# Optimization experiments

Measured on AMD Instinct MI355X. Metric: run time of the kernel, lower is better.

## Reference

```python
import jax, jax.numpy as jnp
import numpy as np

B, S = 2, 1024          # 2 sequences of 1024 tokens (prefill)
HID = 2880
HQ, HKV, D = 64, 8, 64  # query heads, kv heads, head_dim
W = 128                 # sliding window size
THETA = 150000.0
SCALE = D ** -0.5
Q_SIZE, KV_SIZE = HQ * D, HKV * D


def _rope_neox(pos, x):
    # pos: [T] int, x: [T, H, D] -> neox-style full-dim rotary
    half = D // 2
    inv_freq = 1.0 / (THETA ** (jnp.arange(half, dtype=jnp.float32) * 2.0 / D))
    ang = pos.astype(jnp.float32)[:, None] * inv_freq          # [T, D/2]
    cos = jnp.cos(ang)[:, None, :]                             # [T, 1, D/2]
    sin = jnp.sin(ang)[:, None, :]
    x1, x2 = x[..., :half], x[..., half:]
    return jnp.concatenate([x1 * cos - x2 * sin, x1 * sin + x2 * cos], axis=-1)


def setup_inputs() -> dict:
    key = jax.random.key(0)
    ks = jax.random.split(key, 10)
    s = 0.02
    hidden_states = jax.random.normal(ks[0], (B * S, HID), dtype=jnp.float32)
    positions = jnp.tile(jnp.arange(S, dtype=jnp.int32), B)    # per-sequence positions
    Wq = jax.random.normal(ks[1], (HID, Q_SIZE), dtype=jnp.float32) * s
    bq = jax.random.normal(ks[2], (Q_SIZE,), dtype=jnp.float32) * s
    Wk = jax.random.normal(ks[3], (HID, KV_SIZE), dtype=jnp.float32) * s
    bk = jax.random.normal(ks[4], (KV_SIZE,), dtype=jnp.float32) * s
    Wv = jax.random.normal(ks[5], (HID, KV_SIZE), dtype=jnp.float32) * s
    bv = jax.random.normal(ks[6], (KV_SIZE,), dtype=jnp.float32) * s
    Wo = jax.random.normal(ks[7], (Q_SIZE, HID), dtype=jnp.float32) * s
    bo = jax.random.normal(ks[8], (HID,), dtype=jnp.float32) * s
    return {"hidden_states": hidden_states, "positions": positions,
            "Wq": Wq, "bq": bq, "Wk": Wk, "bk": bk,
            "Wv": Wv, "bv": bv, "Wo": Wo, "bo": bo}


def reference(hidden_states, positions, Wq, bq, Wk, bk, Wv, bv, Wo, bo):
    T = hidden_states.shape[0]
    q = (hidden_states @ Wq + bq).reshape(T, HQ, D)
    k = (hidden_states @ Wk + bk).reshape(T, HKV, D)
    v = (hidden_states @ Wv + bv).reshape(T, HKV, D)
    q = _rope_neox(positions, q)
    k = _rope_neox(positions, k)

    # sliding-window causal attention (banded, window = last W keys + self)
    G = HQ // HKV  # GQA group size
    q5 = q.reshape(B, S, HKV, G, D)
    k4 = k.reshape(B, S, HKV, D)
    v4 = v.reshape(B, S, HKV, D)
    offs = jnp.arange(W + 1)
    idx = jnp.arange(S)[:, None] - W + offs[None, :]           # [S, W+1] key index j
    valid = idx >= 0                                           # causal+window band
    idx_c = jnp.clip(idx, 0, S - 1)
    kw = k4[:, idx_c]                                          # [B, S, W+1, HKV, D]
    vw = v4[:, idx_c]
    scores = jnp.einsum('bikgd,biwkd->bikgw', q5, kw) * SCALE  # [B,S,HKV,G,W+1]
    scores = jnp.where(valid[None, :, None, None, :], scores, jnp.float32(-1e30))
    p = jax.nn.softmax(scores, axis=-1)
    o = jnp.einsum('bikgw,biwkd->bikgd', p, vw).reshape(T, Q_SIZE)
    return o @ Wo + bo


if __name__ == '__main__':
    out = reference(**setup_inputs())
    print(out.shape, out.dtype)
```

## Files before the change

kernel.cpp:

```cpp
#include <hip/hip_runtime.h>

#define T_TOK 2048
#define S_LEN 1024
#define HIDN  2880
#define NHQ   64
#define NHKV  8
#define DH    64
#define QSZ   4096
#define KVSZ  512
#define WIN   128
#define NQKV  5120
#define NOPAD 2944

typedef __attribute__((ext_vector_type(4))) float f32x4;
typedef __attribute__((ext_vector_type(8))) short bf16x8;
typedef __attribute__((ext_vector_type(4))) short s16x4;

__device__ __forceinline__ unsigned short f2bf(float f) {
  unsigned u = __float_as_uint(f);
  u += 0x7fffu + ((u >> 16) & 1u);
  return (unsigned short)(u >> 16);
}
__device__ __forceinline__ float bf2f(unsigned short s) {
  return __uint_as_float(((unsigned)s) << 16);
}
__device__ __forceinline__ void ld_g2l16(const void* g, void* l) {
  __builtin_amdgcn_global_load_lds(
      (const __attribute__((address_space(1))) unsigned int*)g,
      (__attribute__((address_space(3))) unsigned int*)l, 16, 0, 0);
}

#define NB_CONV 2880
#define NB_WQ   5760
#define NB_WK   720

__device__ __forceinline__ void transpose_tile(
    const float* __restrict__ W, unsigned short* __restrict__ WT,
    int N, int lbid, float (*tile)[72])
{
  const int tid = threadIdx.x;
  const int nbx = N >> 6;
  const int nb = (lbid % nbx) * 64;
  const int kb = (lbid / nbx) * 32;
  const int kk = tid >> 3;
  const int n8 = (tid & 7) * 8;
  const float* src = W + (size_t)(kb + kk) * N + nb + n8;
  *(f32x4*)&tile[kk][n8]     = *(const f32x4*)(src);
  *(f32x4*)&tile[kk][n8 + 4] = *(const f32x4*)(src + 4);
  __syncthreads();
  const int n  = tid & 63;
  const int k8 = (tid >> 6) * 8;
  bf16x8 p;
  #pragma unroll
  for (int j = 0; j < 8; ++j) p[j] = (short)f2bf(tile[k8 + j][n]);
  *(bf16x8*)(WT + (size_t)(nb + n) * HIDN + kb + k8) = p;
}

__global__ __launch_bounds__(256) void prep_kernel(
    const float* __restrict__ hidden, unsigned short* __restrict__ hbf,
    const float* __restrict__ Wq, const float* __restrict__ Wk,
    const float* __restrict__ Wv, unsigned short* __restrict__ WT)
{
  __shared__ float tile[32][72];
  const int bid = blockIdx.x;
  if (bid < NB_CONV) {
    const size_t off = ((size_t)bid * 256 + threadIdx.x) * 8;
    const f32x4 a = *(const f32x4*)(hidden + off);
    const f32x4 b = *(const f32x4*)(hidden + off + 4);
    bf16x8 p;
    p[0] = (short)f2bf(a[0]); p[1] = (short)f2bf(a[1]);
    p[2] = (short)f2bf(a[2]); p[3] = (short)f2bf(a[3]);
    p[4] = (short)f2bf(b[0]); p[5] = (short)f2bf(b[1]);
    p[6] = (short)f2bf(b[2]); p[7] = (short)f2bf(b[3]);
    *(bf16x8*)(hbf + off) = p;
  } else if (bid < NB_CONV + NB_WQ) {
    transpose_tile(Wq, WT, QSZ, bid - NB_CONV, tile);
  } else if (bid < NB_CONV + NB_WQ + NB_WK) {
    transpose_tile(Wk, WT + (size_t)QSZ * HIDN, KVSZ,
                   bid - NB_CONV - NB_WQ, tile);
  } else {
    transpose_tile(Wv, WT + (size_t)(QSZ + KVSZ) * HIDN, KVSZ,
                   bid - NB_CONV - NB_WQ - NB_WK, tile);
  }
}

__global__ __launch_bounds__(256) void transpose_w(
    const float* __restrict__ W, unsigned short* __restrict__ WT,
    int K, int N)
{
  __shared__ float tile[32][72];
  const int tid = threadIdx.x;
  const int nb = blockIdx.x * 64;
  const int kb = blockIdx.y * 32;
  const int kk = tid >> 3;
  const int n8 = (tid & 7) * 8;
  if (nb + 64 <= N) {
    const float* src = W + (size_t)(kb + kk) * N + nb + n8;
    *(f32x4*)&tile[kk][n8]     = *(const f32x4*)(src);
    *(f32x4*)&tile[kk][n8 + 4] = *(const f32x4*)(src + 4);
  } else {
    #pragma unroll
    for (int u = 0; u < 8; ++u)
      tile[kk][n8 + u] = (nb + n8 + u < N)
          ? W[(size_t)(kb + kk) * N + nb + n8 + u] : 0.f;
  }
  __syncthreads();
  const int n  = tid & 63;
  const int k8 = (tid >> 6) * 8;
  bf16x8 p;
  #pragma unroll
  for (int j = 0; j < 8; ++j) p[j] = (short)f2bf(tile[k8 + j][n]);
  *(bf16x8*)(WT + (size_t)(nb + n) * K + kb + k8) = p;
}

__device__ __forceinline__ void rope_epilogue(
    f32x4 acc[4][4], const float* __restrict__ bias,
    const int* __restrict__ pos, unsigned short* __restrict__ outp,
    int outStride, int colbase, int rowbase, int lane)
{
  const int fr = lane & 15;
  const int r4 = (lane >> 4) * 4;
  const float invf0 = exp2f((float)fr        * (-17.19460283f / 32.0f));
  const float invf1 = exp2f((float)(fr + 16) * (-17.19460283f / 32.0f));
  #pragma unroll
  for (int mt = 0; mt < 4; ++mt) {
    #pragma unroll
    for (int i = 0; i < 4; ++i) {
      const int m = rowbase + mt * 16 + r4 + i;
      const float p = (float)pos[m];
      #pragma unroll
      for (int ntp = 0; ntp < 2; ++ntp) {
        float sv, cv;
        __sincosf(p * (ntp ? invf1 : invf0), &sv, &cv);
        const int c1 = colbase + ntp * 16 + fr;
        const float x1 = acc[mt][ntp][i]     + bias[c1];
        const float x2 = acc[mt][ntp + 2][i] + bias[c1 + 32];
        outp[(size_t)m * outStride + c1]      = f2bf(x1 * cv - x2 * sv);
        outp[(size_t)m * outStride + c1 + 32] = f2bf(x1 * sv + x2 * cv);
      }
    }
  }
}

__global__ __launch_bounds__(256) void gemm_qkv(
    const unsigned short* __restrict__ A, const unsigned short* __restrict__ BT,
    const float* __restrict__ bq, const float* __restrict__ bk,
    const float* __restrict__ bv, const int* __restrict__ pos,
    unsigned short* __restrict__ qb, unsigned short* __restrict__ kb,
    unsigned short* __restrict__ vT)
{
  __shared__ unsigned short As[128 * 64];
  __shared__ unsigned short Bs[128 * 64];
  const int tid  = threadIdx.x;
  const int lane = tid & 63;
  const int wid  = tid >> 6;
  const int wr   = (wid >> 1) * 64;
  const int wc   = (wid & 1) * 64;
  const int m0 = blockIdx.y * 128;
  const int n0 = blockIdx.x * 128;
  const int fr = lane & 15;
  const int fq = lane >> 4;

  f32x4 acc[4][4];
  #pragma unroll
  for (int i = 0; i < 4; ++i)
    #pragma unroll
    for (int j = 0; j < 4; ++j) acc[i][j] = (f32x4){0.f, 0.f, 0.f, 0.f};

  const int rsub = tid >> 3;
  const int cg   = (tid & 7) ^ (rsub & 7);
  const unsigned short* Ap = A  + (size_t)(m0 + rsub) * HIDN + cg * 8;
  const unsigned short* Bp = BT + (size_t)(n0 + rsub) * HIDN + cg * 8;
  const size_t rstep = (size_t)32 * HIDN;

  for (int k0 = 0; k0 < HIDN; k0 += 64) {
    #pragma unroll
    for (int i = 0; i < 4; ++i)
      ld_g2l16(Ap + i * rstep + k0, As + ((size_t)i * 256 + tid) * 8);
    #pragma unroll
    for (int i = 0; i < 4; ++i)
      ld_g2l16(Bp + i * rstep + k0, Bs + ((size_t)i * 256 + tid) * 8);
    __syncthreads();
    #pragma unroll
    for (int ks = 0; ks < 2; ++ks) {
      const int kc = ks * 4 + fq;
      bf16x8 af[4], bfr[4];
      #pragma unroll
      for (int mt = 0; mt < 4; ++mt) {
        const int R = wr + mt * 16 + fr;
        af[mt] = *(const bf16x8*)(As + R * 64 + ((kc ^ (R & 7)) << 3));
      }
      #pragma unroll
      for (int nt = 0; nt < 4; ++nt) {
        const int R = wc + nt * 16 + fr;
        bfr[nt] = *(const bf16x8*)(Bs + R * 64 + ((kc ^ (R & 7)) << 3));
      }
      #pragma unroll
      for (int mt = 0; mt < 4; ++mt)
        #pragma unroll
        for (int nt = 0; nt < 4; ++nt)
          acc[mt][nt] = __builtin_amdgcn_mfma_f32_16x16x32_bf16(
              af[mt], bfr[nt], acc[mt][nt], 0, 0, 0);
    }
    __syncthreads();
  }

  const int r4 = (lane >> 4) * 4;
  if (n0 < QSZ) {
    rope_epilogue(acc, bq, pos, qb, QSZ, n0 + wc, m0 + wr, lane);
  } else if (n0 < QSZ + KVSZ) {
    rope_epilogue(acc, bk, pos, kb, KVSZ, n0 - QSZ + wc, m0 + wr, lane);
  } else {
    #pragma unroll
    for (int nt = 0; nt < 4; ++nt) {
      const int vrow = n0 - (QSZ + KVSZ) + wc + nt * 16 + fr;
      const float bvv = bv[vrow];
      #pragma unroll
      for (int mt = 0; mt < 4; ++mt) {
        const int mb = m0 + wr + mt * 16 + r4;
        s16x4 p;
        p[0] = (short)f2bf(acc[mt][nt][0] + bvv);
        p[1] = (short)f2bf(acc[mt][nt][1] + bvv);
        p[2] = (short)f2bf(acc[mt][nt][2] + bvv);
        p[3] = (short)f2bf(acc[mt][nt][3] + bvv);
        *(s16x4*)(vT + (size_t)vrow * T_TOK + mb) = p;
      }
    }
  }
}

__global__ __launch_bounds__(256) void gemm_o(
    const unsigned short* __restrict__ A, const unsigned short* __restrict__ BT,
    const float* __restrict__ bias, float* __restrict__ C)
{
  __shared__ unsigned short As[128 * 64];
  __shared__ unsigned short Bs[128 * 64];
  const int tid  = threadIdx.x;
  const int lane = tid & 63;
  const int wid  = tid >> 6;
  const int wr   = (wid >> 1) * 64;
  const int wc   = (wid & 1) * 64;
  const int m0 = blockIdx.y * 128;
  const int n0 = blockIdx.x * 128;
  const int fr = lane & 15;
  const int fq = lane >> 4;

  f32x4 acc[4][4];
  #pragma unroll
  for (int i = 0; i < 4; ++i)
    #pragma unroll
    for (int j = 0; j < 4; ++j) acc[i][j] = (f32x4){0.f, 0.f, 0.f, 0.f};

  const int rsub = tid >> 3;
  const int cg   = (tid & 7) ^ (rsub & 7);
  const unsigned short* Ap = A  + (size_t)(m0 + rsub) * QSZ + cg * 8;
  const unsigned short* Bp = BT + (size_t)(n0 + rsub) * QSZ + cg * 8;
  const size_t rstep = (size_t)32 * QSZ;

  for (int k0 = 0; k0 < QSZ; k0 += 64) {
    #pragma unroll
    for (int i = 0; i < 4; ++i)
      ld_g2l16(Ap + i * rstep + k0, As + ((size_t)i * 256 + tid) * 8);
    #pragma unroll
    for (int i = 0; i < 4; ++i)
      ld_g2l16(Bp + i * rstep + k0, Bs + ((size_t)i * 256 + tid) * 8);
    __syncthreads();
    #pragma unroll
    for (int ks = 0; ks < 2; ++ks) {
      const int kc = ks * 4 + fq;
      bf16x8 af[4], bfr[4];
      #pragma unroll
      for (int mt = 0; mt < 4; ++mt) {
        const int R = wr + mt * 16 + fr;
        af[mt] = *(const bf16x8*)(As + R * 64 + ((kc ^ (R & 7)) << 3));
      }
      #pragma unroll
      for (int nt = 0; nt < 4; ++nt) {
        const int R = wc + nt * 16 + fr;
        bfr[nt] = *(const bf16x8*)(Bs + R * 64 + ((kc ^ (R & 7)) << 3));
      }
      #pragma unroll
      for (int mt = 0; mt < 4; ++mt)
        #pragma unroll
        for (int nt = 0; nt < 4; ++nt)
          acc[mt][nt] = __builtin_amdgcn_mfma_f32_16x16x32_bf16(
              af[mt], bfr[nt], acc[mt][nt], 0, 0, 0);
    }
    __syncthreads();
  }

  const int r4 = (lane >> 4) * 4;
  #pragma unroll
  for (int nt = 0; nt < 4; ++nt) {
    const int n = n0 + wc + nt * 16 + fr;
    if (n >= HIDN) continue;
    const float bvv = bias[n];
    #pragma unroll
    for (int mt = 0; mt < 4; ++mt) {
      const int mb = m0 + wr + mt * 16 + r4;
      #pragma unroll
      for (int i = 0; i < 4; ++i)
        C[(size_t)(mb + i) * HIDN + n] = acc[mt][nt][i] + bvv;
    }
  }
}

__global__ __launch_bounds__(256, 3) void attn_kernel(
    const unsigned short* __restrict__ q, const unsigned short* __restrict__ k,
    const unsigned short* __restrict__ vT, unsigned short* __restrict__ o)
{
  __shared__ unsigned short lds[26624];
  unsigned short* Ks = lds;
  unsigned short* Vt = lds;
  unsigned short* Ps = lds + 13824;

  const int tid  = threadIdx.x;
  const int lane = tid & 63;
  const int wid  = tid >> 6;
  const int sq0  = blockIdx.x * 64;
  const int hp   = blockIdx.y;
  const int b    = blockIdx.z;
  const int h0   = hp * 2;
  const int kvh  = hp >> 2;
  const int kp0  = sq0 - WIN;

  const int fr = lane & 15;
  const int fk = (lane >> 4) * 8;
  const int qw = wid * 16;

  bf16x8 qf[2][2];
  {
    const size_t qrow = (size_t)(b * S_LEN + sq0 + qw + fr) * QSZ;
    #pragma unroll
    for (int hh = 0; hh < 2; ++hh)
      #pragma unroll
      for (int ks2 = 0; ks2 < 2; ++ks2)
        qf[hh][ks2] = *(const bf16x8*)(q + qrow + (h0 + hh) * DH + ks2 * 32 + fk);
  }

  #pragma unroll
  for (int j = 0; j < 6; ++j) {
    const int c  = tid + j * 256;
    const int kr = c >> 3, dc = (c & 7) * 8;
    int tok = b * S_LEN + kp0 + kr;
    if (tok < 0) tok = 0;
    const bf16x8 vv = *(const bf16x8*)(k + (size_t)tok * KVSZ + kvh * DH + dc);
    *(bf16x8*)&Ks[kr * 72 + dc] = vv;
  }
  __syncthreads();

  f32x4 S0[12], S1[12];
  #pragma unroll
  for (int i = 0; i < 12; ++i) {
    S0[i] = (f32x4){0.f, 0.f, 0.f, 0.f};
    S1[i] = (f32x4){0.f, 0.f, 0.f, 0.f};
  }
  #pragma unroll
  for (int ks2 = 0; ks2 < 2; ++ks2) {
    #pragma unroll
    for (int nt = 0; nt < 12; ++nt) {
      const bf16x8 bfr = *(const bf16x8*)&Ks[(nt * 16 + fr) * 72 + ks2 * 32 + fk];
      S0[nt] = __builtin_amdgcn_mfma_f32_16x16x32_bf16(qf[0][ks2], bfr, S0[nt], 0, 0, 0);
      S1[nt] = __builtin_amdgcn_mfma_f32_16x16x32_bf16(qf[1][ks2], bfr, S1[nt], 0, 0, 0);
    }
  }

  const int qbase = sq0 + qw + ((lane >> 4) << 2);
  float ls0[4] = {0.f, 0.f, 0.f, 0.f};
  float ls1[4] = {0.f, 0.f, 0.f, 0.f};
  #pragma unroll
  for (int nt = 0; nt < 12; ++nt) {
    const int jpos = kp0 + nt * 16 + fr;
    #pragma unroll
    for (int i = 0; i < 4; ++i) {
      const int qa = qbase + i;
      const bool valid = (jpos >= 0) && (jpos <= qa) && (jpos >= qa - WIN);
      const float e0 = valid ? __expf(S0[nt][i] * 0.125f) : 0.f;
      const float e1 = valid ? __expf(S1[nt][i] * 0.125f) : 0.f;
      S0[nt][i] = e0; ls0[i] += e0;
      S1[nt][i] = e1; ls1[i] += e1;
    }
  }
  #pragma unroll
  for (int off = 1; off < 16; off <<= 1)
    #pragma unroll
    for (int i = 0; i < 4; ++i) {
      ls0[i] += __shfl_xor(ls0[i], off, 64);
      ls1[i] += __shfl_xor(ls1[i], off, 64);
    }
  float inv0[4], inv1[4];
  #pragma unroll
  for (int i = 0; i < 4; ++i) {
    inv0[i] = 1.0f / ls0[i];
    inv1[i] = 1.0f / ls1[i];
  }
  __syncthreads();

  #pragma unroll
  for (int nt = 0; nt < 12; ++nt)
    #pragma unroll
    for (int i = 0; i < 4; ++i)
      Ps[(qbase - sq0 + i) * 200 + nt * 16 + fr] = f2bf(S0[nt][i]);
  if (kp0 >= 0) {
    #pragma unroll
    for (int j = 0; j < 6; ++j) {
      const int c  = tid + j * 256;
      const int dr = c / 24, kc = (c % 24) * 8;
      const bf16x8 vv = *(const bf16x8*)(
          vT + (size_t)(kvh * DH + dr) * T_TOK + b * S_LEN + kp0 + kc);
      *(bf16x8*)&Vt[dr * 200 + kc] = vv;
    }
  } else {
    #pragma unroll
    for (int j = 0; j < 6; ++j) {
      const int c  = tid + j * 256;
      const int dr = c / 24, kc = (c % 24) * 8;
      bf16x8 vv;
      #pragma unroll
      for (int u = 0; u < 8; ++u) {
        int col = b * S_LEN + kp0 + kc + u;
        if (col < 0) col = 0;
        vv[u] = (short)vT[(size_t)(kvh * DH + dr) * T_TOK + col];
      }
      *(bf16x8*)&Vt[dr * 200 + kc] = vv;
    }
  }
  __syncthreads();

  {
    f32x4 O[4];
    #pragma unroll
    for (int i = 0; i < 4; ++i) O[i] = (f32x4){0.f, 0.f, 0.f, 0.f};
    #pragma unroll
    for (int ks2 = 0; ks2 < 6; ++ks2) {
      const bf16x8 pa = *(const bf16x8*)&Ps[(qw + fr) * 200 + ks2 * 32 + fk];
      #pragma unroll
      for (int nt = 0; nt < 4; ++nt) {
        const bf16x8 vb = *(const bf16x8*)&Vt[(nt * 16 + fr) * 200 + ks2 * 32 + fk];
        O[nt] = __builtin_amdgcn_mfma_f32_16x16x32_bf16(pa, vb, O[nt], 0, 0, 0);
      }
    }
    #pragma unroll
    for (int nt = 0; nt < 4; ++nt)
      #pragma unroll
      for (int i = 0; i < 4; ++i)
        o[(size_t)(b * S_LEN + qbase + i) * QSZ + h0 * DH + nt * 16 + fr] =
            f2bf(O[nt][i] * inv0[i]);
  }
  __syncthreads();

  #pragma unroll
  for (int nt = 0; nt < 12; ++nt)
    #pragma unroll
    for (int i = 0; i < 4; ++i)
      Ps[(qbase - sq0 + i) * 200 + nt * 16 + fr] = f2bf(S1[nt][i]);
  __syncthreads();

  {
    f32x4 O[4];
    #pragma unroll
    for (int i = 0; i < 4; ++i) O[i] = (f32x4){0.f, 0.f, 0.f, 0.f};
    #pragma unroll
    for (int ks2 = 0; ks2 < 6; ++ks2) {
      const bf16x8 pa = *(const bf16x8*)&Ps[(qw + fr) * 200 + ks2 * 32 + fk];
      #pragma unroll
      for (int nt = 0; nt < 4; ++nt) {
        const bf16x8 vb = *(const bf16x8*)&Vt[(nt * 16 + fr) * 200 + ks2 * 32 + fk];
        O[nt] = __builtin_amdgcn_mfma_f32_16x16x32_bf16(pa, vb, O[nt], 0, 0, 0);
      }
    }
    #pragma unroll
    for (int nt = 0; nt < 4; ++nt)
      #pragma unroll
      for (int i = 0; i < 4; ++i)
        o[(size_t)(b * S_LEN + qbase + i) * QSZ + (h0 + 1) * DH + nt * 16 + fr] =
            f2bf(O[nt][i] * inv1[i]);
  }
}

extern "C" void kernel_launch(void* const* d_in, const int* in_sizes, int n_in,
                              void* d_out, int out_size, void* d_ws, size_t ws_size,
                              hipStream_t stream) {
  const float* hidden    = (const float*)d_in[0];
  const int*   positions = (const int*)d_in[1];
  const float* Wq = (const float*)d_in[2];
  const float* bq = (const float*)d_in[3];
  const float* Wk = (const float*)d_in[4];
  const float* bk = (const float*)d_in[5];
  const float* Wv = (const float*)d_in[6];
  const float* bv = (const float*)d_in[7];
  const float* Wo = (const float*)d_in[8];
  const float* bo = (const float*)d_in[9];
  float* out = (float*)d_out;

  char* ws = (char*)d_ws;
  unsigned short* hbf   = (unsigned short*)(ws);
  unsigned short* WqkvT = (unsigned short*)(ws + 11796480);
  unsigned short* qb    = (unsigned short*)(ws + 41287680);
  unsigned short* kb    = (unsigned short*)(ws + 58064896);
  unsigned short* vTb   = (unsigned short*)(ws + 60162048);

  prep_kernel<<<dim3(NB_CONV + NB_WQ + 2 * NB_WK), dim3(256), 0, stream>>>(
      hidden, hbf, Wq, Wk, Wv, WqkvT);

  gemm_qkv<<<dim3(NQKV / 128, T_TOK / 128), dim3(256), 0, stream>>>(
      hbf, WqkvT, bq, bk, bv, positions, qb, kb, vTb);

  transpose_w<<<dim3(NOPAD / 64, QSZ / 32), dim3(256), 0, stream>>>(
      Wo, WqkvT, QSZ, HIDN);

  attn_kernel<<<dim3(S_LEN / 64, NHQ / 2, 2), dim3(256), 0, stream>>>(
      qb, kb, vTb, qb);
  gemm_o<<<dim3(NOPAD / 128, T_TOK / 128), dim3(256), 0, stream>>>(
      qb, WqkvT, bo, out);
}
```

Baseline: 375.0 us.

## Rewrite QKV GEMM as 256x256 tile, 8-wave, double-buffered pipelined kernel

```diff
diff --git a/kernel.cpp b/kernel.cpp
--- a/kernel.cpp
+++ b/kernel.cpp
@@ -11,6 +11,7 @@
 #define WIN   128
 #define NQKV  5120
 #define NOPAD 2944
+#define NT    45
 
 typedef __attribute__((ext_vector_type(4))) float f32x4;
 typedef __attribute__((ext_vector_type(8))) short bf16x8;
@@ -113,8 +114,8 @@
   *(bf16x8*)(WT + (size_t)(nb + n) * K + kb + k8) = p;
 }
 
-__device__ __forceinline__ void rope_epilogue(
-    f32x4 acc[4][4], const float* __restrict__ bias,
+__device__ __forceinline__ void rope_epilogue8(
+    f32x4 (*acc)[4], const float* __restrict__ bias,
     const int* __restrict__ pos, unsigned short* __restrict__ outp,
     int outStride, int colbase, int rowbase, int lane)
 {
@@ -123,7 +124,7 @@
   const float invf0 = exp2f((float)fr        * (-17.19460283f / 32.0f));
   const float invf1 = exp2f((float)(fr + 16) * (-17.19460283f / 32.0f));
   #pragma unroll
-  for (int mt = 0; mt < 4; ++mt) {
+  for (int mt = 0; mt < 8; ++mt) {
     #pragma unroll
     for (int i = 0; i < 4; ++i) {
       const int m = rowbase + mt * 16 + r4 + i;
@@ -142,82 +143,128 @@
   }
 }
 
-__global__ __launch_bounds__(256) void gemm_qkv(
+__global__ __launch_bounds__(512, 2) void gemm_qkv(
     const unsigned short* __restrict__ A, const unsigned short* __restrict__ BT,
     const float* __restrict__ bq, const float* __restrict__ bk,
     const float* __restrict__ bv, const int* __restrict__ pos,
     unsigned short* __restrict__ qb, unsigned short* __restrict__ kb,
     unsigned short* __restrict__ vT)
 {
-  __shared__ unsigned short As[128 * 64];
-  __shared__ unsigned short Bs[128 * 64];
+  __shared__ unsigned short lds[65536];
   const int tid  = threadIdx.x;
   const int lane = tid & 63;
   const int wid  = tid >> 6;
-  const int wr   = (wid >> 1) * 64;
-  const int wc   = (wid & 1) * 64;
-  const int m0 = blockIdx.y * 128;
-  const int n0 = blockIdx.x * 128;
+  const int wm   = wid >> 2;
+  const int wn   = wid & 3;
+  const int bid  = blockIdx.x;
+  const int wg   = (bid & 7) * 20 + (bid >> 3);
+  const int n0   = (wg % 20) * 256;
+  const int m0   = (wg / 20) * 256;
   const int fr = lane & 15;
   const int fq = lane >> 4;
 
-  f32x4 acc[4][4];
-  #pragma unroll
-  for (int i = 0; i < 4; ++i)
-    #pragma unroll
-    for (int j = 0; j < 4; ++j) acc[i][j] = (f32x4){0.f, 0.f, 0.f, 0.f};
-
   const int rsub = tid >> 3;
   const int cg   = (tid & 7) ^ (rsub & 7);
-  const unsigned short* Ap = A  + (size_t)(m0 + rsub) * HIDN + cg * 8;
-  const unsigned short* Bp = BT + (size_t)(n0 + rsub) * HIDN + cg * 8;
-  const size_t rstep = (size_t)32 * HIDN;
-
-  for (int k0 = 0; k0 < HIDN; k0 += 64) {
-    #pragma unroll
-    for (int i = 0; i < 4; ++i)
-      ld_g2l16(Ap + i * rstep + k0, As + ((size_t)i * 256 + tid) * 8);
-    #pragma unroll
-    for (int i = 0; i < 4; ++i)
-      ld_g2l16(Bp + i * rstep + k0, Bs + ((size_t)i * 256 + tid) * 8);
-    __syncthreads();
-    #pragma unroll
-    for (int ks = 0; ks < 2; ++ks) {
-      const int kc = ks * 4 + fq;
-      bf16x8 af[4], bfr[4];
-      #pragma unroll
-      for (int mt = 0; mt < 4; ++mt) {
-        const int R = wr + mt * 16 + fr;
-        af[mt] = *(const bf16x8*)(As + R * 64 + ((kc ^ (R & 7)) << 3));
-      }
-      #pragma unroll
-      for (int nt = 0; nt < 4; ++nt) {
-        const int R = wc + nt * 16 + fr;
-        bfr[nt] = *(const bf16x8*)(Bs + R * 64 + ((kc ^ (R & 7)) << 3));
-      }
-      #pragma unroll
-      for (int mt = 0; mt < 4; ++mt)
+  const unsigned short* Asrc = A  + (size_t)(m0 + rsub) * HIDN + cg * 8;
+  const unsigned short* Bsrc = BT + (size_t)(n0 + rsub) * HIDN + cg * 8;
+  const size_t half_step = (size_t)128 * HIDN;
+  const size_t r64 = (size_t)64 * HIDN;
+
+  #define STAGE(src, slot)                                         \
+    do {                                                           \
+      ld_g2l16((src),       (slot) + (size_t)tid * 8);             \
+      ld_g2l16((src) + r64, (slot) + (size_t)(512 + tid) * 8);     \
+    } while (0)
+
+  STAGE(Bsrc,                  lds + 16384);
+  STAGE(Bsrc + half_step,      lds + 24576);
+  STAGE(Asrc,                  lds + 0);
+  STAGE(Asrc + half_step,      lds + 8192);
+  STAGE(Bsrc + 64,             lds + 32768 + 16384);
+  STAGE(Bsrc + half_step + 64, lds + 32768 + 24576);
+  STAGE(Asrc + 64,             lds + 32768 + 0);
+  STAGE(Asrc + half_step + 64, lds + 32768 + 8192);
+  asm volatile("s_waitcnt vmcnt(8)" ::: "memory");
+  __builtin_amdgcn_s_barrier();
+
+  f32x4 acc[8][4];
+  #pragma unroll
+  for (int i = 0; i < 8; ++i)
+    #pragma unroll
+    for (int j = 0; j < 4; ++j) acc[i][j] = (f32x4){0.f, 0.f, 0.f, 0.f};
+  bf16x8 bfr[4][2];
+
+  for (int t = 0; t < NT; ++t) {
+    unsigned short* Abuf = lds + (t & 1) * 32768;
+    unsigned short* Bbuf = Abuf + 16384;
+    unsigned short* nAbuf = lds + ((t + 1) & 1) * 32768;
+    const int kA = (t + 1) * 64;
+    const int kB = (t + 2) * 64;
+    #pragma unroll
+    for (int q = 0; q < 4; ++q) {
+      if (q == 0) {
         #pragma unroll
-        for (int nt = 0; nt < 4; ++nt)
-          acc[mt][nt] = __builtin_amdgcn_mfma_f32_16x16x32_bf16(
-              af[mt], bfr[nt], acc[mt][nt], 0, 0, 0);
-    }
-    __syncthreads();
-  }
-
-  const int r4 = (lane >> 4) * 4;
-  if (n0 < QSZ) {
-    rope_epilogue(acc, bq, pos, qb, QSZ, n0 + wc, m0 + wr, lane);
-  } else if (n0 < QSZ + KVSZ) {
-    rope_epilogue(acc, bk, pos, kb, KVSZ, n0 - QSZ + wc, m0 + wr, lane);
+        for (int nf = 0; nf < 4; ++nf)
+          #pragma unroll
+          for (int ks = 0; ks < 2; ++ks) {
+            const int R = wn * 64 + nf * 16 + fr;
+            const int kc = ks * 4 + fq;
+            bfr[nf][ks] = *(const bf16x8*)(Bbuf + R * 64 + ((kc ^ (R & 7)) << 3));
+          }
+      }
+      bf16x8 af[2][2];
+      #pragma unroll
+      for (int j = 0; j < 2; ++j)
+        #pragma unroll
+        for (int ks = 0; ks < 2; ++ks) {
+          const int R = wm * 128 + (q * 2 + j) * 16 + fr;
+          const int kc = ks * 4 + fq;
+          af[j][ks] = *(const bf16x8*)(Abuf + R * 64 + ((kc ^ (R & 7)) << 3));
+        }
+      if (q == 0) {
+        if (t >= 1 && t <= NT - 2) STAGE(Asrc + kA, nAbuf);
+      } else if (q == 1) {
+        if (t >= 1 && t <= NT - 2) STAGE(Asrc + half_step + kA, nAbuf + 8192);
+      } else if (q == 2) {
+        if (t <= NT - 3) STAGE(Bsrc + kB, Bbuf);
+      } else {
+        if (t <= NT - 3) STAGE(Bsrc + half_step + kB, Bbuf + 8192);
+      }
+      if (q == 3) {
+        if (t < NT - 2)       asm volatile("s_waitcnt vmcnt(4)" ::: "memory");
+        else if (t == NT - 2) asm volatile("s_waitcnt vmcnt(0)" ::: "memory");
+      }
+      __builtin_amdgcn_s_barrier();
+      __builtin_amdgcn_s_setprio(1);
+      #pragma unroll
+      for (int j = 0; j < 2; ++j)
+        #pragma unroll
+        for (int nf = 0; nf < 4; ++nf)
+          #pragma unroll
+          for (int ks = 0; ks < 2; ++ks)
+            acc[q * 2 + j][nf] = __builtin_amdgcn_mfma_f32_16x16x32_bf16(
+                af[j][ks], bfr[nf][ks], acc[q * 2 + j][nf], 0, 0, 0);
+      __builtin_amdgcn_s_setprio(0);
+      __builtin_amdgcn_s_barrier();
+    }
+  }
+  #undef STAGE
+
+  const int cb = n0 + wn * 64;
+  const int rowbase = m0 + wm * 128;
+  if (cb < QSZ) {
+    rope_epilogue8(acc, bq, pos, qb, QSZ, cb, rowbase, lane);
+  } else if (cb < QSZ + KVSZ) {
+    rope_epilogue8(acc, bk, pos, kb, KVSZ, cb - QSZ, rowbase, lane);
   } else {
+    const int r4 = (lane >> 4) * 4;
     #pragma unroll
     for (int nt = 0; nt < 4; ++nt) {
-      const int vrow = n0 - (QSZ + KVSZ) + wc + nt * 16 + fr;
+      const int vrow = cb - (QSZ + KVSZ) + nt * 16 + fr;
       const float bvv = bv[vrow];
       #pragma unroll
-      for (int mt = 0; mt < 4; ++mt) {
-        const int mb = m0 + wr + mt * 16 + r4;
+      for (int mt = 0; mt < 8; ++mt) {
+        const int mb = rowbase + mt * 16 + r4;
         s16x4 p;
         p[0] = (short)f2bf(acc[mt][nt][0] + bvv);
         p[1] = (short)f2bf(acc[mt][nt][1] + bvv);
@@ -503,7 +550,7 @@
   prep_kernel<<<dim3(NB_CONV + NB_WQ + 2 * NB_WK), dim3(256), 0, stream>>>(
       hidden, hbf, Wq, Wk, Wv, WqkvT);
 
-  gemm_qkv<<<dim3(NQKV / 128, T_TOK / 128), dim3(256), 0, stream>>>(
+  gemm_qkv<<<dim3((NQKV / 256) * (T_TOK / 256)), dim3(512), 0, stream>>>(
       hbf, WqkvT, bq, bk, bv, positions, qb, kb, vTb);
 
   transpose_w<<<dim3(NOPAD / 64, QSZ / 32), dim3(256), 0, stream>>>(
```

Result: faster. 359.4 us (-4.1%).
